# Performance work log

Measured on AMD Instinct MI355X. Metric: run time of the kernel, lower is better.

The kernel has to match this reference:

```python
import jax, jax.numpy as jnp
import numpy as np

N = 40000
E = 200000
D = 32
NUM_BANDS = 3
ORDER = 4
EPS = 1e-8
LN_EPS = 1e-5


def setup_inputs() -> dict:
    key = jax.random.key(0)
    ks = jax.random.split(key, 20)
    h = jax.random.normal(ks[0], (N, D), dtype=jnp.float32)
    Q = jax.random.normal(ks[1], (E, D, D), dtype=jnp.float32) / jnp.sqrt(jnp.float32(D))
    edge_index = jax.random.randint(ks[2], (2, E), 0, N, dtype=jnp.int32)
    coeffs = jnp.ones((NUM_BANDS, ORDER + 1), dtype=jnp.float32) / (ORDER + 1)
    s = 1.0 / np.sqrt(D)
    proj_W = jax.random.uniform(ks[3], (NUM_BANDS, D, D), minval=-s, maxval=s, dtype=jnp.float32)
    proj_b = jax.random.uniform(ks[4], (NUM_BANDS, D), minval=-s, maxval=s, dtype=jnp.float32)
    proj_g = jnp.ones((NUM_BANDS, D), dtype=jnp.float32)
    proj_beta = jnp.zeros((NUM_BANDS, D), dtype=jnp.float32)
    s3 = 1.0 / np.sqrt(NUM_BANDS * D)
    fus_W1 = jax.random.uniform(ks[5], (NUM_BANDS * D, D), minval=-s3, maxval=s3, dtype=jnp.float32)
    fus_b1 = jax.random.uniform(ks[6], (D,), minval=-s3, maxval=s3, dtype=jnp.float32)
    fus_g = jnp.ones((D,), dtype=jnp.float32)
    fus_beta = jnp.zeros((D,), dtype=jnp.float32)
    fus_W2 = jax.random.uniform(ks[7], (D, D), minval=-s, maxval=s, dtype=jnp.float32)
    fus_b2 = jax.random.uniform(ks[8], (D,), minval=-s, maxval=s, dtype=jnp.float32)
    return {"h": h, "Q": Q, "edge_index": edge_index, "coeffs": coeffs,
            "proj_W": proj_W, "proj_b": proj_b, "proj_g": proj_g, "proj_beta": proj_beta,
            "fus_W1": fus_W1, "fus_b1": fus_b1, "fus_g": fus_g, "fus_beta": fus_beta,
            "fus_W2": fus_W2, "fus_b2": fus_b2}


def _layer_norm(x, g, b):
    mu = x.mean(-1, keepdims=True)
    var = x.var(-1, keepdims=True)  # biased, as torch LayerNorm
    return (x - mu) / jnp.sqrt(var + LN_EPS) * g + b


def reference(h, Q, edge_index, coeffs, proj_W, proj_b, proj_g, proj_beta,
              fus_W1, fus_b1, fus_g, fus_beta, fus_W2, fus_b2):
    row, col = edge_index[0], edge_index[1]
    n = h.shape[0]
    ones_e = jnp.ones(row.shape[0], dtype=h.dtype)
    deg = (jax.ops.segment_sum(ones_e, row, num_segments=n)
           + jax.ops.segment_sum(ones_e, col, num_segments=n))  # [N]

    def matvec(x):
        # gather -> per-edge DxD bmm -> scatter_add; diag via degree
        Qh = jnp.einsum('eij,ej->ei', Q, x[col])          # [E, D]
        off = jax.ops.segment_sum(Qh, row, num_segments=n)  # [N, D]
        return deg[:, None] * x - off

    # power iteration for lambda_max (5 iters, fixed key for determinism)
    v = jax.random.normal(jax.random.key(42), h.shape, dtype=h.dtype)
    v = v / jnp.linalg.norm(v)
    lam = jnp.array(1.0, dtype=h.dtype)
    for _ in range(5):
        Lv = matvec(v)
        lam = (v * Lv).sum() / ((v * v).sum() + EPS)
        v = Lv / (jnp.linalg.norm(Lv) + EPS)
    lam = jnp.maximum(lam, 1.0)

    def L_tilde(x):
        return 2.0 / (lam + EPS) * matvec(x) - x

    bands = []
    for b_idx in range(NUM_BANDS):
        w = jax.nn.softmax(coeffs[b_idx])
        T_prev = h
        T_curr = L_tilde(h)
        res = w[0] * T_prev + w[1] * T_curr
        for k in range(2, ORDER + 1):
            T_next = 2.0 * L_tilde(T_curr) - T_prev
            res = res + w[k] * T_next
            T_prev, T_curr = T_curr, T_next
        p = jax.nn.silu(_layer_norm(res @ proj_W[b_idx] + proj_b[b_idx],
                                    proj_g[b_idx], proj_beta[b_idx]))
        bands.append(p)

    cat = jnp.concatenate(bands, axis=-1)  # [N, 3D]
    fused = jax.nn.silu(_layer_norm(cat @ fus_W1 + fus_b1, fus_g, fus_beta)) @ fus_W2 + fus_b2
    return h + fused
```

## Files before the change

### kernel.cpp

```cpp
#include <hip/hip_runtime.h>
#include <hip/hip_fp16.h>
#include <math.h>

#define NN 40000
#define EE 200000
#define DD 32
#define ND (NN * DD)
#define LNEPS 1e-5f

typedef float    fv4 __attribute__((ext_vector_type(4)));
typedef unsigned uv4 __attribute__((ext_vector_type(4)));

#define SLOT_S1    0
#define SLOT_S2    32
#define SLOT_ALPHA 48

__device__ __forceinline__ void threefry2x32(unsigned k0, unsigned k1,
                                             unsigned x0, unsigned x1,
                                             unsigned& o0, unsigned& o1) {
  const unsigned k2 = k0 ^ k1 ^ 0x1BD11BDAu;
  unsigned v0 = x0 + k0, v1 = x1 + k1;
#define TF_ROUND(r) { v0 += v1; v1 = (v1 << (r)) | (v1 >> (32 - (r))); v1 ^= v0; }
  TF_ROUND(13) TF_ROUND(15) TF_ROUND(26) TF_ROUND(6)
  v0 += k1; v1 += k2 + 1u;
  TF_ROUND(17) TF_ROUND(29) TF_ROUND(16) TF_ROUND(24)
  v0 += k2; v1 += k0 + 2u;
  TF_ROUND(13) TF_ROUND(15) TF_ROUND(26) TF_ROUND(6)
  v0 += k0; v1 += k1 + 3u;
  TF_ROUND(17) TF_ROUND(29) TF_ROUND(16) TF_ROUND(24)
  v0 += k1; v1 += k2 + 4u;
  TF_ROUND(13) TF_ROUND(15) TF_ROUND(26) TF_ROUND(6)
  v0 += k2; v1 += k0 + 5u;
#undef TF_ROUND
  o0 = v0; o1 = v1;
}

__device__ __forceinline__ float wave64_sum(float x) {
  for (int o = 32; o > 0; o >>= 1) x += __shfl_xor(x, o, 64);
  return x;
}
__device__ __forceinline__ float g32_sum(float x) {
  for (int o = 16; o > 0; o >>= 1) x += __shfl_xor(x, o, 32);
  return x;
}

__global__ void k_deg(const int* __restrict__ ei, float* __restrict__ deg,
                      int* __restrict__ hist) {
  int e = blockIdx.x * 256 + threadIdx.x;
  if (e < EE) {
    int r = ei[e];
    atomicAdd(deg + r, 1.0f);
    atomicAdd(deg + ei[EE + e], 1.0f);
    atomicAdd(hist + r, 1);
  }
}

__global__ __launch_bounds__(1024) void k_scan(const int* __restrict__ hist,
                                               int* __restrict__ row_start,
                                               int* __restrict__ cursor) {
  __shared__ int part[1024];
  const int t = threadIdx.x;
  const int base = t * 40;
  int s = 0;
  for (int i = base; i < base + 40 && i < NN; ++i) s += hist[i];
  part[t] = s;
  __syncthreads();
  for (int off = 1; off < 1024; off <<= 1) {
    int v = (t >= off) ? part[t - off] : 0;
    __syncthreads();
    part[t] += v;
    __syncthreads();
  }
  int ex = (t == 0) ? 0 : part[t - 1];
  for (int i = base; i < base + 40 && i < NN; ++i) {
    row_start[i] = ex;
    cursor[i] = ex;
    ex += hist[i];
  }
  if (t == 0) row_start[NN] = EE;
}

__global__ void k_genv(float* __restrict__ v) {
  int i = blockIdx.x * 256 + threadIdx.x;
  unsigned o0, o1;
  threefry2x32(0u, 42u, 0u, (unsigned)i, o0, o1);
  unsigned bits = o1;
  float f = __uint_as_float((bits >> 9) | 0x3f800000u) - 1.0f;
  const float lo = -0.99999994f;
  float u = fmaxf(lo, f * 2.0f + lo);
  v[i] = 1.41421354f * erfinvf(u);
}

__device__ __forceinline__ int clamp8(float q) {
  int v = (int)rintf(q);
  return v < -127 ? -127 : (v > 127 ? 127 : v);
}
__device__ __forceinline__ unsigned pack4v(fv4 q, float inv) {
  int q0 = clamp8(q.x * inv), q1 = clamp8(q.y * inv),
      q2 = clamp8(q.z * inv), q3 = clamp8(q.w * inv);
  return (q0 & 255) | ((q1 & 255) << 8) | ((q2 & 255) << 16) | ((q3 & 255) << 24);
}
__device__ __forceinline__ void dp4(unsigned u, fv4 xv, float& acc) {
  acc = fmaf((float)(signed char)(u),        xv.x, acc);
  acc = fmaf((float)(signed char)(u >> 8),   xv.y, acc);
  acc = fmaf((float)(signed char)(u >> 16),  xv.z, acc);
  acc = fmaf((float)(signed char)(u >> 24),  xv.w, acc);
}

__global__ __launch_bounds__(256) void k_cvt(const float* __restrict__ Q,
                                             const int* __restrict__ ei,
                                             int* __restrict__ cursor,
                                             char* __restrict__ Qi8,
                                             __half* __restrict__ Qs,
                                             int* __restrict__ cols) {
  const int slot = threadIdx.x >> 5;
  const int lane = threadIdx.x & 31;
  const int e = blockIdx.x * 8 + slot;
  const int row = ei[e];
  const int col = ei[EE + e];
  int pos = 0;
  if (lane == 0) pos = atomicAdd(cursor + row, 1);
  pos = __shfl(pos, 0, 32);
  const fv4* __restrict__ q4 =
      (const fv4*)(Q + (size_t)e * (DD * DD) + (size_t)lane * DD);
  fv4 qf[8];
#pragma unroll
  for (int k = 0; k < 8; ++k) qf[k] = __builtin_nontemporal_load(q4 + k);
  float m = 0.0f;
#pragma unroll
  for (int k = 0; k < 8; ++k) {
    m = fmaxf(m, fmaxf(fmaxf(fabsf(qf[k].x), fabsf(qf[k].y)),
                       fmaxf(fabsf(qf[k].z), fabsf(qf[k].w))));
  }
  __half sh = __float2half(m * (1.0f / 127.0f));
  float s = __half2float(sh);
  float inv = (s > 0.0f) ? 1.0f / s : 0.0f;
  uv4 pa, pb;
  pa.x = pack4v(qf[0], inv); pa.y = pack4v(qf[1], inv);
  pa.z = pack4v(qf[2], inv); pa.w = pack4v(qf[3], inv);
  pb.x = pack4v(qf[4], inv); pb.y = pack4v(qf[5], inv);
  pb.z = pack4v(qf[6], inv); pb.w = pack4v(qf[7], inv);
  uv4* __restrict__ qs = (uv4*)(Qi8 + (size_t)pos * (DD * DD) + (size_t)lane * DD);
  qs[0] = pa;
  qs[1] = pb;
  Qs[pos * DD + lane] = sh;
  if (lane == 0) cols[pos] = col;
}

#define CHUNK 16

__global__ __launch_bounds__(256) void k_gather(const float* __restrict__ x,
                                                const float* __restrict__ xprev,
                                                const char* __restrict__ Qi8,
                                                const __half* __restrict__ Qs,
                                                const int* __restrict__ cols,
                                                const int* __restrict__ row_start,
                                                const float* __restrict__ deg,
                                                const float* __restrict__ scal,
                                                float* __restrict__ out, int mode) {
  __shared__ float lds[4][CHUNK][DD];
  const int wid  = threadIdx.x >> 6;
  const int lane = threadIdx.x & 63;
  const int half = lane >> 5;
  const int d    = lane & 31;
  const int r = blockIdx.x * 4 + wid;
  const int beg = row_start[r];
  const int end = row_start[r + 1];
  const int degree = end - beg;

  float acc = 0.0f;
  for (int chunk = 0; chunk < degree; chunk += CHUNK) {
    const int nchunk = min(CHUNK, degree - chunk);
    int myc = (lane < nchunk) ? cols[beg + chunk + lane] : 0;
    {
      const int el = lane >> 2;
      const int pt = lane & 3;
      if (el < nchunk) {
        const int c = __shfl(myc, el, 64);
        const fv4* __restrict__ xs = (const fv4*)(x + (size_t)c * DD);
        fv4 a = xs[pt * 2];
        fv4 b = xs[pt * 2 + 1];
        fv4* __restrict__ dst = (fv4*)&lds[wid][el][pt * 8];
        dst[0] = a;
        dst[1] = b;
      }
    }
    uv4 qa = {0, 0, 0, 0}, qb = {0, 0, 0, 0};
    float sc = 0.0f;
    {
      const int p = half;
      if (p < nchunk) {
        const size_t pos = (size_t)(beg + chunk + p);
        const uv4* __restrict__ q8 = (const uv4*)(Qi8 + pos * (DD * DD) + (size_t)d * DD);
        qa = q8[0];
        qb = q8[1];
        sc = __half2float(Qs[pos * DD + d]);
      }
    }
    for (int p0 = 0; p0 < nchunk; p0 += 2) {
      const int pn = p0 + 2 + half;
      uv4 na = {0, 0, 0, 0}, nb = {0, 0, 0, 0};
      float ns = 0.0f;
      if (pn < nchunk) {
        const size_t pos = (size_t)(beg + chunk + pn);
        const uv4* __restrict__ q8 = (const uv4*)(Qi8 + pos * (DD * DD) + (size_t)d * DD);
        na = q8[0];
        nb = q8[1];
        ns = __half2float(Qs[pos * DD + d]);
      }
      const int p = p0 + half;
      if (p < nchunk) {
        const fv4* __restrict__ xl = (const fv4*)&lds[wid][p][0];
        fv4 xr[8];
#pragma unroll
        for (int k = 0; k < 8; ++k) xr[k] = xl[k];
        float dot = 0.0f;
        dp4(qa.x, xr[0], dot); dp4(qa.y, xr[1], dot);
        dp4(qa.z, xr[2], dot); dp4(qa.w, xr[3], dot);
        dp4(qb.x, xr[4], dot); dp4(qb.y, xr[5], dot);
        dp4(qb.z, xr[6], dot); dp4(qb.w, xr[7], dot);
        acc = fmaf(sc, dot, acc);
      }
      qa = na; qb = nb; sc = ns;
    }
  }
  acc += __shfl_xor(acc, 32, 64);

  if (half == 0) {
    const size_t idx = (size_t)r * DD + d;
    const float xi = x[idx];
    const float dv = deg[r];
    float o;
    if (mode == 0)      o = dv * xi - acc;
    else if (mode == 1) o = scal[SLOT_ALPHA] * (dv * xi - acc) - xi;
    else                o = 2.0f * scal[SLOT_ALPHA] * (dv * xi - acc)
                            - 2.0f * xi - xprev[idx];
    out[idx] = o;
  }
}

__global__ void k_pre(const float* __restrict__ x, const float* __restrict__ xprev,
                      const float* __restrict__ deg, const float* __restrict__ scal,
                      float* __restrict__ out, int mode) {
  int i = blockIdx.x * 256 + threadIdx.x;
  float d = deg[i >> 5];
  float xi = x[i];
  if (mode == 0)       out[i] = d * xi;
  else if (mode == 1)  out[i] = scal[SLOT_ALPHA] * d * xi - xi;
  else                 out[i] = 2.0f * scal[SLOT_ALPHA] * d * xi - 2.0f * xi - xprev[i];
}

__global__ __launch_bounds__(256) void k_matvec(const float* __restrict__ x,
                                                const float* __restrict__ Q,
                                                const int* __restrict__ ei,
                                                float* __restrict__ out,
                                                const float* __restrict__ scal,
                                                int use_alpha, float smul) {
  const int slot = threadIdx.x >> 5;
  const int lane = threadIdx.x & 31;
  const int e = blockIdx.x * 8 + slot;
  const float factor = use_alpha ? scal[SLOT_ALPHA] * smul : smul;
  const int row = ei[e];
  const int col = ei[EE + e];
  const fv4* __restrict__ x4 = (const fv4*)(x + (size_t)col * DD);
  fv4 xr[8];
#pragma unroll
  for (int k = 0; k < 8; ++k) xr[k] = x4[k];
  const fv4* __restrict__ q4 =
      (const fv4*)(Q + (size_t)e * (DD * DD) + (size_t)lane * DD);
  float acc = 0.0f;
#pragma unroll
  for (int k = 0; k < 8; ++k) {
    fv4 q = q4[k];
    acc = fmaf(q.x, xr[k].x, acc);
    acc = fmaf(q.y, xr[k].y, acc);
    acc = fmaf(q.z, xr[k].z, acc);
    acc = fmaf(q.w, xr[k].w, acc);
  }
  atomicAdd(out + (size_t)row * DD + lane, -factor * acc);
}

#define DOT_BLOCKS 640
__global__ void k_dots(const float* __restrict__ u4, const float* __restrict__ u5,
                       float* __restrict__ scal) {
  float s1 = 0.0f, s2 = 0.0f;
  for (int i = blockIdx.x * 256 + threadIdx.x; i < ND; i += DOT_BLOCKS * 256) {
    float a = u4[i], b = u5[i];
    s1 = fmaf(a, b, s1);
    s2 = fmaf(a, a, s2);
  }
  s1 = wave64_sum(s1);
  s2 = wave64_sum(s2);
  __shared__ float ls1[4], ls2[4];
  int w = threadIdx.x >> 6;
  if ((threadIdx.x & 63) == 0) { ls1[w] = s1; ls2[w] = s2; }
  __syncthreads();
  if (threadIdx.x == 0) {
    atomicAdd(scal + SLOT_S1, ls1[0] + ls1[1] + ls1[2] + ls1[3]);
    atomicAdd(scal + SLOT_S2, ls2[0] + ls2[1] + ls2[2] + ls2[3]);
  }
}

__global__ void k_alpha(float* __restrict__ scal) {
  float lam = scal[SLOT_S1] / scal[SLOT_S2] / (1.0f + 1e-8f);
  lam = fmaxf(lam, 1.0f);
  scal[SLOT_ALPHA] = 2.0f / (lam + 1e-8f);
}

__global__ __launch_bounds__(256) void k_fuse(
    const float* __restrict__ h,
    const float* __restrict__ T1, const float* __restrict__ T2,
    const float* __restrict__ T3, const float* __restrict__ T4,
    const float* __restrict__ coeffs,
    const float* __restrict__ projW, const float* __restrict__ projb,
    const float* __restrict__ projg, const float* __restrict__ projbeta,
    const float* __restrict__ fusW1, const float* __restrict__ fusb1,
    const float* __restrict__ fusg, const float* __restrict__ fusbeta,
    const float* __restrict__ fusW2, const float* __restrict__ fusb2,
    float* __restrict__ out) {
  __shared__ float s_res[8][3][DD];
  __shared__ float s_p[8][3 * DD];
  __shared__ float s_s[8][DD];
  const int slot = threadIdx.x >> 5;
  const int lane = threadIdx.x & 31;
  const int n = blockIdx.x * 8 + slot;

  float w[3][5];
#pragma unroll
  for (int b = 0; b < 3; ++b) {
    float m = -1e30f;
#pragma unroll
    for (int k = 0; k < 5; ++k) m = fmaxf(m, coeffs[b * 5 + k]);
    float s = 0.0f;
#pragma unroll
    for (int k = 0; k < 5; ++k) { w[b][k] = expf(coeffs[b * 5 + k] - m); s += w[b][k]; }
#pragma unroll
    for (int k = 0; k < 5; ++k) w[b][k] /= s;
  }

  const int idx = n * DD + lane;
  float hd = h[idx], t1 = T1[idx], t2 = T2[idx], t3 = T3[idx], t4 = T4[idx];
#pragma unroll
  for (int b = 0; b < 3; ++b)
    s_res[slot][b][lane] =
        w[b][0] * hd + w[b][1] * t1 + w[b][2] * t2 + w[b][3] * t3 + w[b][4] * t4;
  __syncthreads();

#pragma unroll
  for (int b = 0; b < 3; ++b) {
    float y = projb[b * DD + lane];
#pragma unroll
    for (int j = 0; j < DD; ++j)
      y = fmaf(s_res[slot][b][j], projW[(b * DD + j) * DD + lane], y);
    float mu = g32_sum(y) * (1.0f / DD);
    float d = y - mu;
    float var = g32_sum(d * d) * (1.0f / DD);
    float z = d * rsqrtf(var + LNEPS) * projg[b * DD + lane] + projbeta[b * DD + lane];
    float pb = z / (1.0f + expf(-z));
    s_p[slot][b * DD + lane] = pb;
  }
  __syncthreads();

  float y = fusb1[lane];
#pragma unroll
  for (int j = 0; j < 3 * DD; ++j)
    y = fmaf(s_p[slot][j], fusW1[j * DD + lane], y);
  float mu = g32_sum(y) * (1.0f / DD);
  float d = y - mu;
  float var = g32_sum(d * d) * (1.0f / DD);
  float z = d * rsqrtf(var + LNEPS) * fusg[lane] + fusbeta[lane];
  float sv = z / (1.0f + expf(-z));
  s_s[slot][lane] = sv;
  __syncthreads();

  float o = fusb2[lane];
#pragma unroll
  for (int j = 0; j < DD; ++j)
    o = fmaf(s_s[slot][j], fusW2[j * DD + lane], o);
  out[idx] = hd + o;
}

extern "C" void kernel_launch(void* const* d_in, const int* in_sizes, int n_in,
                              void* d_out, int out_size, void* d_ws, size_t ws_size,
                              hipStream_t stream) {
  (void)in_sizes; (void)n_in; (void)out_size;
  const float* h        = (const float*)d_in[0];
  const float* Q        = (const float*)d_in[1];
  const int*   ei       = (const int*)d_in[2];
  const float* coeffs   = (const float*)d_in[3];
  const float* projW    = (const float*)d_in[4];
  const float* projb    = (const float*)d_in[5];
  const float* projg    = (const float*)d_in[6];
  const float* projbeta = (const float*)d_in[7];
  const float* fusW1    = (const float*)d_in[8];
  const float* fusb1    = (const float*)d_in[9];
  const float* fusg     = (const float*)d_in[10];
  const float* fusbeta  = (const float*)d_in[11];
  const float* fusW2    = (const float*)d_in[12];
  const float* fusb2    = (const float*)d_in[13];
  float* out = (float*)d_out;

  const size_t qi_bytes  = (size_t)EE * DD * DD;
  const size_t qs_bytes  = (size_t)EE * DD * sizeof(__half);
  const size_t col_bytes = (size_t)EE * sizeof(int);
  const size_t idx_bytes = (size_t)(3 * NN + 2) * sizeof(int);
  const size_t f32_elems = 6u * (size_t)ND + NN + 64;
  const size_t need = qi_bytes + qs_bytes + col_bytes + idx_bytes +
                      f32_elems * sizeof(float) + 256;
  const bool fast = ws_size >= need;

  char*   Qi8 = (char*)d_ws;
  __half* Qs  = (__half*)((char*)d_ws + qi_bytes);
  int*  cols      = (int*)((char*)d_ws + qi_bytes + qs_bytes);
  int*  row_start = cols + EE;
  int*  cursor    = row_start + NN + 1;
  float* base = fast
      ? (float*)((char*)d_ws + ((qi_bytes + qs_bytes + col_bytes + idx_bytes + 255) & ~(size_t)255))
      : (float*)d_ws;
  float* uA   = base;
  float* uB   = uA + ND;
  float* T1   = uB + ND;
  float* T2   = T1 + ND;
  float* T3   = T2 + ND;
  float* T4   = T3 + ND;
  float* deg  = T4 + ND;
  float* scal = deg + NN;
  int*   hist = (int*)(scal + 64);

  (void)hipMemsetAsync(deg, 0, (2 * NN + 64) * sizeof(float), stream);

  k_deg<<<(EE + 255) / 256, 256, 0, stream>>>(ei, deg, hist);
  k_genv<<<ND / 256, 256, 0, stream>>>(uA);

  if (fast) {
    k_scan<<<1, 1024, 0, stream>>>(hist, row_start, cursor);
    k_cvt<<<EE / 8, 256, 0, stream>>>(Q, ei, cursor, Qi8, Qs, cols);

    float* cur = uA;
    float* nxt = uB;
    for (int it = 0; it < 5; ++it) {
      k_gather<<<NN / 4, 256, 0, stream>>>(cur, nullptr, Qi8, Qs, cols,
                                           row_start, deg, scal, nxt, 0);
      float* t = cur; cur = nxt; nxt = t;
    }
    k_dots<<<DOT_BLOCKS, 256, 0, stream>>>(nxt, cur, scal);
    k_alpha<<<1, 1, 0, stream>>>(scal);

    const float* xin[4]   = {h, T1, T2, T3};
    const float* prevs[4] = {nullptr, h, T1, T2};
    float* touts[4]       = {T1, T2, T3, T4};
    for (int k = 0; k < 4; ++k) {
      k_gather<<<NN / 4, 256, 0, stream>>>(xin[k], prevs[k], Qi8, Qs, cols,
                                           row_start, deg, scal, touts[k],
                                           k == 0 ? 1 : 2);
    }
  } else {
    float* cur = uA;
    float* nxt = uB;
    for (int it = 0; it < 5; ++it) {
      k_pre<<<ND / 256, 256, 0, stream>>>(cur, nullptr, deg, scal, nxt, 0);
      k_matvec<<<EE / 8, 256, 0, stream>>>(cur, Q, ei, nxt, scal, 0, 1.0f);
      float* t = cur; cur = nxt; nxt = t;
    }
    k_dots<<<DOT_BLOCKS, 256, 0, stream>>>(nxt, cur, scal);
    k_alpha<<<1, 1, 0, stream>>>(scal);
    const float* xin[4]   = {h, T1, T2, T3};
    const float* prevs[4] = {nullptr, h, T1, T2};
    float* touts[4]       = {T1, T2, T3, T4};
    for (int k = 0; k < 4; ++k) {
      k_pre<<<ND / 256, 256, 0, stream>>>(xin[k], prevs[k], deg, scal, touts[k],
                                          k == 0 ? 1 : 2);
      k_matvec<<<EE / 8, 256, 0, stream>>>(xin[k], Q, ei, touts[k], scal, 1,
                                           k == 0 ? 1.0f : 2.0f);
    }
  }

  k_fuse<<<NN / 8, 256, 0, stream>>>(h, T1, T2, T3, T4, coeffs,
                                     projW, projb, projg, projbeta,
                                     fusW1, fusb1, fusg, fusbeta,
                                     fusW2, fusb2, out);
}
```

Before: 950.9 us.

## Fuse power iteration and Chebyshev sweeps into persistent kernels with grid barriers

Replaces eleven separate gather launches plus the dot and alpha kernels with two persistent kernels of 1024 blocks. Each kernel loops over rows in a grid-stride pattern and separates dependent sweeps with a hierarchical atomic grid barrier. The dot-product reduction and lambda computation are folded into the power kernel. This removes launch overhead and tail idle time between passes, but requires all 1024 blocks to be co-resident, adds spin-wait barrier cost, and the barrier gives up after a fixed spin count instead of failing.

```diff
diff --git a/kernel.cpp b/kernel.cpp
--- a/kernel.cpp
+++ b/kernel.cpp
@@ -7,13 +7,13 @@
 #define DD 32
 #define ND (NN * DD)
 #define LNEPS 1e-5f
+#define GRID 1024
 
 typedef float    fv4 __attribute__((ext_vector_type(4)));
 typedef unsigned uv4 __attribute__((ext_vector_type(4)));
 
-#define SLOT_S1    0
-#define SLOT_S2    32
 #define SLOT_ALPHA 48
+#define SCAL_FLOATS (64 + 2048 + 64)
 
 __device__ __forceinline__ void threefry2x32(unsigned k0, unsigned k1,
                                              unsigned x0, unsigned x1,
@@ -44,6 +44,41 @@
   return x;
 }
 
+__device__ __forceinline__ void gbar(int* bar) {
+  __syncthreads();
+  if (threadIdx.x == 0) {
+    __threadfence();
+    int* gen = bar + 33 * 32;
+    int g = __hip_atomic_load(gen, __ATOMIC_RELAXED, __HIP_MEMORY_SCOPE_AGENT);
+    const int leaf = blockIdx.x & 31;
+    int c = __hip_atomic_fetch_add(bar + leaf * 32, 1, __ATOMIC_ACQ_REL,
+                                   __HIP_MEMORY_SCOPE_AGENT);
+    bool done = false;
+    if (c == (GRID / 32) - 1) {
+      __hip_atomic_store(bar + leaf * 32, 0, __ATOMIC_RELAXED,
+                         __HIP_MEMORY_SCOPE_AGENT);
+      int rc = __hip_atomic_fetch_add(bar + 32 * 32, 1, __ATOMIC_ACQ_REL,
+                                      __HIP_MEMORY_SCOPE_AGENT);
+      if (rc == 31) {
+        __hip_atomic_store(bar + 32 * 32, 0, __ATOMIC_RELAXED,
+                           __HIP_MEMORY_SCOPE_AGENT);
+        __hip_atomic_store(gen, g + 1, __ATOMIC_RELEASE,
+                           __HIP_MEMORY_SCOPE_AGENT);
+        done = true;
+      }
+    }
+    if (!done) {
+      long long spins = 0;
+      while (__hip_atomic_load(gen, __ATOMIC_ACQUIRE,
+                               __HIP_MEMORY_SCOPE_AGENT) == g) {
+        __builtin_amdgcn_s_sleep(2);
+        if (++spins > 200000000LL) break;
+      }
+    }
+  }
+  __syncthreads();
+}
+
 __global__ void k_deg(const int* __restrict__ ei, float* __restrict__ deg,
                       int* __restrict__ hist) {
   int e = blockIdx.x * 256 + threadIdx.x;
@@ -149,93 +184,175 @@
 
 #define CHUNK 16
 
-__global__ __launch_bounds__(256) void k_gather(const float* __restrict__ x,
-                                                const float* __restrict__ xprev,
-                                                const char* __restrict__ Qi8,
-                                                const __half* __restrict__ Qs,
-                                                const int* __restrict__ cols,
-                                                const int* __restrict__ row_start,
-                                                const float* __restrict__ deg,
-                                                const float* __restrict__ scal,
-                                                float* __restrict__ out, int mode) {
-  __shared__ float lds[4][CHUNK][DD];
-  const int wid  = threadIdx.x >> 6;
+__device__ __forceinline__ void sweep_rows(const float* __restrict__ x,
+                                           const float* __restrict__ xprev,
+                                           const char* __restrict__ Qi8,
+                                           const __half* __restrict__ Qs,
+                                           const int* __restrict__ cols,
+                                           const int* __restrict__ row_start,
+                                           const float* __restrict__ deg,
+                                           float alpha,
+                                           float* __restrict__ out, int mode,
+                                           float (*ldsw)[DD]) {
   const int lane = threadIdx.x & 63;
   const int half = lane >> 5;
   const int d    = lane & 31;
-  const int r = blockIdx.x * 4 + wid;
-  const int beg = row_start[r];
-  const int end = row_start[r + 1];
-  const int degree = end - beg;
-
-  float acc = 0.0f;
-  for (int chunk = 0; chunk < degree; chunk += CHUNK) {
-    const int nchunk = min(CHUNK, degree - chunk);
-    int myc = (lane < nchunk) ? cols[beg + chunk + lane] : 0;
-    {
-      const int el = lane >> 2;
-      const int pt = lane & 3;
-      if (el < nchunk) {
-        const int c = __shfl(myc, el, 64);
-        const fv4* __restrict__ xs = (const fv4*)(x + (size_t)c * DD);
-        fv4 a = xs[pt * 2];
-        fv4 b = xs[pt * 2 + 1];
-        fv4* __restrict__ dst = (fv4*)&lds[wid][el][pt * 8];
-        dst[0] = a;
-        dst[1] = b;
+  const int wid  = threadIdx.x >> 6;
+  for (int r = blockIdx.x * 4 + wid; r < NN; r += GRID * 4) {
+    const int beg = row_start[r];
+    const int end = row_start[r + 1];
+    const int degree = end - beg;
+    float acc = 0.0f;
+    for (int chunk = 0; chunk < degree; chunk += CHUNK) {
+      const int nchunk = min(CHUNK, degree - chunk);
+      int myc = (lane < nchunk) ? cols[beg + chunk + lane] : 0;
+      {
+        const int el = lane >> 2;
+        const int pt = lane & 3;
+        if (el < nchunk) {
+          const int c = __shfl(myc, el, 64);
+          const fv4* __restrict__ xs = (const fv4*)(x + (size_t)c * DD);
+          fv4 a = xs[pt * 2];
+          fv4 b = xs[pt * 2 + 1];
+          fv4* __restrict__ dst = (fv4*)&ldsw[el][pt * 8];
+          dst[0] = a;
+          dst[1] = b;
+        }
       }
-    }
-    uv4 qa = {0, 0, 0, 0}, qb = {0, 0, 0, 0};
-    float sc = 0.0f;
-    {
-      const int p = half;
-      if (p < nchunk) {
-        const size_t pos = (size_t)(beg + chunk + p);
-        const uv4* __restrict__ q8 = (const uv4*)(Qi8 + pos * (DD * DD) + (size_t)d * DD);
-        qa = q8[0];
-        qb = q8[1];
-        sc = __half2float(Qs[pos * DD + d]);
+      uv4 qa = {0, 0, 0, 0}, qb = {0, 0, 0, 0};
+      float sc = 0.0f;
+      {
+        const int p = half;
+        if (p < nchunk) {
+          const size_t pos = (size_t)(beg + chunk + p);
+          const uv4* __restrict__ q8 =
+              (const uv4*)(Qi8 + pos * (DD * DD) + (size_t)d * DD);
+          qa = q8[0];
+          qb = q8[1];
+          sc = __half2float(Qs[pos * DD + d]);
+        }
       }
-    }
-    for (int p0 = 0; p0 < nchunk; p0 += 2) {
-      const int pn = p0 + 2 + half;
-      uv4 na = {0, 0, 0, 0}, nb = {0, 0, 0, 0};
-      float ns = 0.0f;
-      if (pn < nchunk) {
-        const size_t pos = (size_t)(beg + chunk + pn);
-        const uv4* __restrict__ q8 = (const uv4*)(Qi8 + pos * (DD * DD) + (size_t)d * DD);
-        na = q8[0];
-        nb = q8[1];
-        ns = __half2float(Qs[pos * DD + d]);
+      for (int p0 = 0; p0 < nchunk; p0 += 2) {
+        const int pn = p0 + 2 + half;
+        uv4 na = {0, 0, 0, 0}, nb = {0, 0, 0, 0};
+        float ns = 0.0f;
+        if (pn < nchunk) {
+          const size_t pos = (size_t)(beg + chunk + pn);
+          const uv4* __restrict__ q8 =
+              (const uv4*)(Qi8 + pos * (DD * DD) + (size_t)d * DD);
+          na = q8[0];
+          nb = q8[1];
+          ns = __half2float(Qs[pos * DD + d]);
+        }
+        const int p = p0 + half;
+        if (p < nchunk) {
+          const fv4* __restrict__ xl = (const fv4*)&ldsw[p][0];
+          fv4 xr[8];
+#pragma unroll
+          for (int k = 0; k < 8; ++k) xr[k] = xl[k];
+          float dot = 0.0f;
+          dp4(qa.x, xr[0], dot); dp4(qa.y, xr[1], dot);
+          dp4(qa.z, xr[2], dot); dp4(qa.w, xr[3], dot);
+          dp4(qb.x, xr[4], dot); dp4(qb.y, xr[5], dot);
+          dp4(qb.z, xr[6], dot); dp4(qb.w, xr[7], dot);
+          acc = fmaf(sc, dot, acc);
+        }
+        qa = na; qb = nb; sc = ns;
       }
-      const int p = p0 + half;
-      if (p < nchunk) {
-        const fv4* __restrict__ xl = (const fv4*)&lds[wid][p][0];
-        fv4 xr[8];
-#pragma unroll
-        for (int k = 0; k < 8; ++k) xr[k] = xl[k];
-        float dot = 0.0f;
-        dp4(qa.x, xr[0], dot); dp4(qa.y, xr[1], dot);
-        dp4(qa.z, xr[2], dot); dp4(qa.w, xr[3], dot);
-        dp4(qb.x, xr[4], dot); dp4(qb.y, xr[5], dot);
-        dp4(qb.z, xr[6], dot); dp4(qb.w, xr[7], dot);
-        acc = fmaf(sc, dot, acc);
-      }
-      qa = na; qb = nb; sc = ns;
-    }
-  }
-  acc += __shfl_xor(acc, 32, 64);
-
-  if (half == 0) {
-    const size_t idx = (size_t)r * DD + d;
-    const float xi = x[idx];
-    const float dv = deg[r];
-    float o;
-    if (mode == 0)      o = dv * xi - acc;
-    else if (mode == 1) o = scal[SLOT_ALPHA] * (dv * xi - acc) - xi;
-    else                o = 2.0f * scal[SLOT_ALPHA] * (dv * xi - acc)
-                            - 2.0f * xi - xprev[idx];
-    out[idx] = o;
+    }
+    acc += __shfl_xor(acc, 32, 64);
+    if (half == 0) {
+      const size_t idx = (size_t)r * DD + d;
+      const float xi = x[idx];
+      const float dv = deg[r];
+      float o;
+      if (mode == 0)      o = dv * xi - acc;
+      else if (mode == 1) o = alpha * (dv * xi - acc) - xi;
+      else                o = 2.0f * alpha * (dv * xi - acc) - 2.0f * xi - xprev[idx];
+      out[idx] = o;
+    }
+  }
+}
+
+__global__ __launch_bounds__(256, 4) void k_power(const char* __restrict__ Qi8,
+                                                  const __half* __restrict__ Qs,
+                                                  const int* __restrict__ cols,
+                                                  const int* __restrict__ row_start,
+                                                  const float* __restrict__ deg,
+                                                  float* __restrict__ uA,
+                                                  float* __restrict__ uB,
+                                                  float* __restrict__ scal,
+                                                  int* __restrict__ bar) {
+  __shared__ float lds[4][CHUNK][DD];
+  float (*ldsw)[DD] = lds[threadIdx.x >> 6];
+
+  const float* src[5] = {uA, uB, uA, uB, uA};
+  float*       dst[5] = {uB, uA, uB, uA, uB};
+#pragma unroll
+  for (int s = 0; s < 5; ++s) {
+    sweep_rows(src[s], uA, Qi8, Qs, cols, row_start, deg, 0.0f, dst[s], 0, ldsw);
+    gbar(bar);
+  }
+  float s1 = 0.0f, s2 = 0.0f;
+  for (int i = blockIdx.x * 256 + threadIdx.x; i < ND; i += GRID * 256) {
+    float a = uA[i], b = uB[i];
+    s1 = fmaf(a, b, s1);
+    s2 = fmaf(a, a, s2);
+  }
+  s1 = wave64_sum(s1);
+  s2 = wave64_sum(s2);
+  __shared__ float ls1[4], ls2[4];
+  int w = threadIdx.x >> 6;
+  if ((threadIdx.x & 63) == 0) { ls1[w] = s1; ls2[w] = s2; }
+  __syncthreads();
+  if (threadIdx.x == 0) {
+    const int leaf = blockIdx.x & 31;
+    float b1 = ls1[0] + ls1[1] + ls1[2] + ls1[3];
+    float b2 = ls2[0] + ls2[1] + ls2[2] + ls2[3];
+    __hip_atomic_fetch_add(scal + 64 + leaf * 32, b1, __ATOMIC_RELAXED,
+                           __HIP_MEMORY_SCOPE_AGENT);
+    __hip_atomic_fetch_add(scal + 64 + 1024 + leaf * 32, b2, __ATOMIC_RELAXED,
+                           __HIP_MEMORY_SCOPE_AGENT);
+  }
+  gbar(bar);
+  if (blockIdx.x == 0 && threadIdx.x == 0) {
+    float S1 = 0.0f, S2 = 0.0f;
+    for (int l = 0; l < 32; ++l) {
+      S1 += __hip_atomic_load(scal + 64 + l * 32, __ATOMIC_ACQUIRE,
+                              __HIP_MEMORY_SCOPE_AGENT);
+      S2 += __hip_atomic_load(scal + 64 + 1024 + l * 32, __ATOMIC_ACQUIRE,
+                              __HIP_MEMORY_SCOPE_AGENT);
+    }
+    float lam = S1 / S2 / (1.0f + 1e-8f);
+    lam = fmaxf(lam, 1.0f);
+    scal[SLOT_ALPHA] = 2.0f / (lam + 1e-8f);
+  }
+}
+
+__global__ __launch_bounds__(256, 4) void k_cheb4(const float* __restrict__ h,
+                                                  const char* __restrict__ Qi8,
+                                                  const __half* __restrict__ Qs,
+                                                  const int* __restrict__ cols,
+                                                  const int* __restrict__ row_start,
+                                                  const float* __restrict__ deg,
+                                                  const float* __restrict__ scal,
+                                                  float* __restrict__ T1,
+                                                  float* __restrict__ T2,
+                                                  float* __restrict__ T3,
+                                                  float* __restrict__ T4,
+                                                  int* __restrict__ bar) {
+  __shared__ float lds[4][CHUNK][DD];
+  float (*ldsw)[DD] = lds[threadIdx.x >> 6];
+  const float alpha = scal[SLOT_ALPHA];
+
+  const float* xin[4] = {h, T1, T2, T3};
+  const float* prv[4] = {h, h, T1, T2};
+  float*      outs[4] = {T1, T2, T3, T4};
+#pragma unroll
+  for (int k = 0; k < 4; ++k) {
+    sweep_rows(xin[k], prv[k], Qi8, Qs, cols, row_start, deg, alpha, outs[k],
+               k == 0 ? 1 : 2, ldsw);
+    if (k < 3) gbar(bar);
   }
 }
 
@@ -296,13 +413,13 @@
   if ((threadIdx.x & 63) == 0) { ls1[w] = s1; ls2[w] = s2; }
   __syncthreads();
   if (threadIdx.x == 0) {
-    atomicAdd(scal + SLOT_S1, ls1[0] + ls1[1] + ls1[2] + ls1[3]);
-    atomicAdd(scal + SLOT_S2, ls2[0] + ls2[1] + ls2[2] + ls2[3]);
+    atomicAdd(scal + 64, ls1[0] + ls1[1] + ls1[2] + ls1[3]);
+    atomicAdd(scal + 64 + 1024, ls2[0] + ls2[1] + ls2[2] + ls2[3]);
   }
 }
 
 __global__ void k_alpha(float* __restrict__ scal) {
-  float lam = scal[SLOT_S1] / scal[SLOT_S2] / (1.0f + 1e-8f);
+  float lam = scal[64] / scal[64 + 1024] / (1.0f + 1e-8f);
   lam = fmaxf(lam, 1.0f);
   scal[SLOT_ALPHA] = 2.0f / (lam + 1e-8f);
 }
@@ -404,9 +521,10 @@
   const size_t qs_bytes  = (size_t)EE * DD * sizeof(__half);
   const size_t col_bytes = (size_t)EE * sizeof(int);
   const size_t idx_bytes = (size_t)(3 * NN + 2) * sizeof(int);
-  const size_t f32_elems = 6u * (size_t)ND + NN + 64;
-  const size_t need = qi_bytes + qs_bytes + col_bytes + idx_bytes +
-                      f32_elems * sizeof(float) + 256;
+  const size_t BAR_INTS  = 34 * 32 + 64;
+  const size_t f32_elems = 6u * (size_t)ND + NN + SCAL_FLOATS;
+  const size_t meta = qi_bytes + qs_bytes + col_bytes + idx_bytes;
+  const size_t need = meta + (f32_elems + NN + BAR_INTS) * sizeof(float) + 512;
   const bool fast = ws_size >= need;
 
   char*   Qi8 = (char*)d_ws;
@@ -415,7 +533,7 @@
   int*  row_start = cols + EE;
   int*  cursor    = row_start + NN + 1;
   float* base = fast
-      ? (float*)((char*)d_ws + ((qi_bytes + qs_bytes + col_bytes + idx_bytes + 255) & ~(size_t)255))
+      ? (float*)((char*)d_ws + ((meta + 255) & ~(size_t)255))
       : (float*)d_ws;
   float* uA   = base;
   float* uB   = uA + ND;
@@ -425,9 +543,12 @@
   float* T4   = T3 + ND;
   float* deg  = T4 + ND;
   float* scal = deg + NN;
-  int*   hist = (int*)(scal + 64);
-
-  (void)hipMemsetAsync(deg, 0, (2 * NN + 64) * sizeof(float), stream);
+  int*   hist = (int*)(scal + SCAL_FLOATS);
+  int*   bar  = hist + NN;
+
+  (void)hipMemsetAsync(deg, 0,
+                       (2 * (size_t)NN + SCAL_FLOATS + BAR_INTS) * sizeof(float),
+                       stream);
 
   k_deg<<<(EE + 255) / 256, 256, 0, stream>>>(ei, deg, hist);
   k_genv<<<ND / 256, 256, 0, stream>>>(uA);
@@ -435,25 +556,10 @@
   if (fast) {
     k_scan<<<1, 1024, 0, stream>>>(hist, row_start, cursor);
     k_cvt<<<EE / 8, 256, 0, stream>>>(Q, ei, cursor, Qi8, Qs, cols);
-
-    float* cur = uA;
-    float* nxt = uB;
-    for (int it = 0; it < 5; ++it) {
-      k_gather<<<NN / 4, 256, 0, stream>>>(cur, nullptr, Qi8, Qs, cols,
-                                           row_start, deg, scal, nxt, 0);
-      float* t = cur; cur = nxt; nxt = t;
-    }
-    k_dots<<<DOT_BLOCKS, 256, 0, stream>>>(nxt, cur, scal);
-    k_alpha<<<1, 1, 0, stream>>>(scal);
-
-    const float* xin[4]   = {h, T1, T2, T3};
-    const float* prevs[4] = {nullptr, h, T1, T2};
-    float* touts[4]       = {T1, T2, T3, T4};
-    for (int k = 0; k < 4; ++k) {
-      k_gather<<<NN / 4, 256, 0, stream>>>(xin[k], prevs[k], Qi8, Qs, cols,
-                                           row_start, deg, scal, touts[k],
-                                           k == 0 ? 1 : 2);
-    }
+    k_power<<<GRID, 256, 0, stream>>>(Qi8, Qs, cols, row_start, deg, uA, uB,
+                                      scal, bar);
+    k_cheb4<<<GRID, 256, 0, stream>>>(h, Qi8, Qs, cols, row_start, deg, scal,
+                                      T1, T2, T3, T4, bar);
   } else {
     float* cur = uA;
     float* nxt = uB;
```

Result: slower. 2.288 ms (+140.6%).

## Fuse first power-iteration matvec into Q quantization pass and deepen Q prefetch

Applied to the files above, without the earlier changes.

The first power-iteration matvec is computed inside the Q conversion kernel using the fp32 Q already loaded, scattering results with atomics into a buffer pre-initialized by k_pre. This removes one gather pass over the quantized Q. The gather kernel now prefetches Q two edges ahead and hoists per-row loads before the loop. The cost is extra x gathers and atomics in the conversion kernel, plus higher register pressure in the gather.

```diff
diff --git a/kernel.cpp b/kernel.cpp
--- a/kernel.cpp
+++ b/kernel.cpp
@@ -107,12 +107,14 @@
   acc = fmaf((float)(signed char)(u >> 24),  xv.w, acc);
 }
 
-__global__ __launch_bounds__(256) void k_cvt(const float* __restrict__ Q,
-                                             const int* __restrict__ ei,
-                                             int* __restrict__ cursor,
-                                             char* __restrict__ Qi8,
-                                             __half* __restrict__ Qs,
-                                             int* __restrict__ cols) {
+__global__ __launch_bounds__(256) void k_cvt_mv(const float* __restrict__ x,
+                                                const float* __restrict__ Q,
+                                                const int* __restrict__ ei,
+                                                int* __restrict__ cursor,
+                                                char* __restrict__ Qi8,
+                                                __half* __restrict__ Qs,
+                                                int* __restrict__ cols,
+                                                float* __restrict__ out) {
   const int slot = threadIdx.x >> 5;
   const int lane = threadIdx.x & 31;
   const int e = blockIdx.x * 8 + slot;
@@ -121,11 +123,23 @@
   int pos = 0;
   if (lane == 0) pos = atomicAdd(cursor + row, 1);
   pos = __shfl(pos, 0, 32);
+  const fv4* __restrict__ x4 = (const fv4*)(x + (size_t)col * DD);
+  fv4 xr[8];
+#pragma unroll
+  for (int k = 0; k < 8; ++k) xr[k] = x4[k];
   const fv4* __restrict__ q4 =
       (const fv4*)(Q + (size_t)e * (DD * DD) + (size_t)lane * DD);
   fv4 qf[8];
 #pragma unroll
   for (int k = 0; k < 8; ++k) qf[k] = __builtin_nontemporal_load(q4 + k);
+  float acc = 0.0f;
+#pragma unroll
+  for (int k = 0; k < 8; ++k) {
+    acc = fmaf(qf[k].x, xr[k].x, acc);
+    acc = fmaf(qf[k].y, xr[k].y, acc);
+    acc = fmaf(qf[k].z, xr[k].z, acc);
+    acc = fmaf(qf[k].w, xr[k].w, acc);
+  }
   float m = 0.0f;
 #pragma unroll
   for (int k = 0; k < 8; ++k) {
@@ -145,6 +159,7 @@
   qs[1] = pb;
   Qs[pos * DD + lane] = sh;
   if (lane == 0) cols[pos] = col;
+  atomicAdd(out + (size_t)row * DD + lane, -acc);
 }
 
 #define CHUNK 16
@@ -168,6 +183,11 @@
   const int end = row_start[r + 1];
   const int degree = end - beg;
 
+  const size_t idx = (size_t)r * DD + d;
+  const float xi = x[idx];
+  const float dv = deg[r];
+  const float xp = (mode == 2) ? xprev[idx] : 0.0f;
+
   float acc = 0.0f;
   for (int chunk = 0; chunk < degree; chunk += CHUNK) {
     const int nchunk = min(CHUNK, degree - chunk);
@@ -185,29 +205,22 @@
         dst[1] = b;
       }
     }
-    uv4 qa = {0, 0, 0, 0}, qb = {0, 0, 0, 0};
-    float sc = 0.0f;
-    {
-      const int p = half;
-      if (p < nchunk) {
-        const size_t pos = (size_t)(beg + chunk + p);
-        const uv4* __restrict__ q8 = (const uv4*)(Qi8 + pos * (DD * DD) + (size_t)d * DD);
-        qa = q8[0];
-        qb = q8[1];
-        sc = __half2float(Qs[pos * DD + d]);
-      }
-    }
+    uv4 a0 = {0,0,0,0}, b0 = {0,0,0,0}, a1 = {0,0,0,0}, b1 = {0,0,0,0};
+    float s0 = 0.0f, s1 = 0.0f;
+#define LOADQ(PP, A, B, S)                                                    \
+    if ((PP) < nchunk) {                                                      \
+      const size_t pos = (size_t)(beg + chunk + (PP));                        \
+      const uv4* __restrict__ q8 =                                            \
+          (const uv4*)(Qi8 + pos * (DD * DD) + (size_t)d * DD);               \
+      A = q8[0]; B = q8[1];                                                   \
+      S = __half2float(Qs[pos * DD + d]);                                     \
+    }
+    LOADQ(half, a0, b0, s0)
+    LOADQ(2 + half, a1, b1, s1)
     for (int p0 = 0; p0 < nchunk; p0 += 2) {
-      const int pn = p0 + 2 + half;
-      uv4 na = {0, 0, 0, 0}, nb = {0, 0, 0, 0};
-      float ns = 0.0f;
-      if (pn < nchunk) {
-        const size_t pos = (size_t)(beg + chunk + pn);
-        const uv4* __restrict__ q8 = (const uv4*)(Qi8 + pos * (DD * DD) + (size_t)d * DD);
-        na = q8[0];
-        nb = q8[1];
-        ns = __half2float(Qs[pos * DD + d]);
-      }
+      uv4 a2 = {0,0,0,0}, b2 = {0,0,0,0};
+      float s2 = 0.0f;
+      LOADQ(p0 + 4 + half, a2, b2, s2)
       const int p = p0 + half;
       if (p < nchunk) {
         const fv4* __restrict__ xl = (const fv4*)&lds[wid][p][0];
@@ -215,26 +228,25 @@
 #pragma unroll
         for (int k = 0; k < 8; ++k) xr[k] = xl[k];
         float dot = 0.0f;
-        dp4(qa.x, xr[0], dot); dp4(qa.y, xr[1], dot);
-        dp4(qa.z, xr[2], dot); dp4(qa.w, xr[3], dot);
-        dp4(qb.x, xr[4], dot); dp4(qb.y, xr[5], dot);
-        dp4(qb.z, xr[6], dot); dp4(qb.w, xr[7], dot);
-        acc = fmaf(sc, dot, acc);
+        dp4(a0.x, xr[0], dot); dp4(a0.y, xr[1], dot);
+        dp4(a0.z, xr[2], dot); dp4(a0.w, xr[3], dot);
+        dp4(b0.x, xr[4], dot); dp4(b0.y, xr[5], dot);
+        dp4(b0.z, xr[6], dot); dp4(b0.w, xr[7], dot);
+        acc = fmaf(s0, dot, acc);
       }
-      qa = na; qb = nb; sc = ns;
-    }
+      a0 = a1; b0 = b1; s0 = s1;
+      a1 = a2; b1 = b2; s1 = s2;
+    }
+#undef LOADQ
   }
   acc += __shfl_xor(acc, 32, 64);
 
   if (half == 0) {
-    const size_t idx = (size_t)r * DD + d;
-    const float xi = x[idx];
-    const float dv = deg[r];
     float o;
     if (mode == 0)      o = dv * xi - acc;
     else if (mode == 1) o = scal[SLOT_ALPHA] * (dv * xi - acc) - xi;
     else                o = 2.0f * scal[SLOT_ALPHA] * (dv * xi - acc)
-                            - 2.0f * xi - xprev[idx];
+                            - 2.0f * xi - xp;
     out[idx] = o;
   }
 }
@@ -404,9 +416,9 @@
   const size_t qs_bytes  = (size_t)EE * DD * sizeof(__half);
   const size_t col_bytes = (size_t)EE * sizeof(int);
   const size_t idx_bytes = (size_t)(3 * NN + 2) * sizeof(int);
-  const size_t f32_elems = 6u * (size_t)ND + NN + 64;
-  const size_t need = qi_bytes + qs_bytes + col_bytes + idx_bytes +
-                      f32_elems * sizeof(float) + 256;
+  const size_t f32_elems = 6u * (size_t)ND + 2u * NN + 64;
+  const size_t meta = qi_bytes + qs_bytes + col_bytes + idx_bytes;
+  const size_t need = meta + f32_elems * sizeof(float) + 512;
   const bool fast = ws_size >= need;
 
   char*   Qi8 = (char*)d_ws;
@@ -415,7 +427,7 @@
   int*  row_start = cols + EE;
   int*  cursor    = row_start + NN + 1;
   float* base = fast
-      ? (float*)((char*)d_ws + ((qi_bytes + qs_bytes + col_bytes + idx_bytes + 255) & ~(size_t)255))
+      ? (float*)((char*)d_ws + ((meta + 255) & ~(size_t)255))
       : (float*)d_ws;
   float* uA   = base;
   float* uB   = uA + ND;
@@ -427,27 +439,29 @@
   float* scal = deg + NN;
   int*   hist = (int*)(scal + 64);
 
-  (void)hipMemsetAsync(deg, 0, (2 * NN + 64) * sizeof(float), stream);
+  (void)hipMemsetAsync(deg, 0, (2 * (size_t)NN + 64) * sizeof(float), stream);
 
   k_deg<<<(EE + 255) / 256, 256, 0, stream>>>(ei, deg, hist);
   k_genv<<<ND / 256, 256, 0, stream>>>(uA);
 
   if (fast) {
     k_scan<<<1, 1024, 0, stream>>>(hist, row_start, cursor);
-    k_cvt<<<EE / 8, 256, 0, stream>>>(Q, ei, cursor, Qi8, Qs, cols);
-
-    float* cur = uA;
-    float* nxt = uB;
-    for (int it = 0; it < 5; ++it) {
-      k_gather<<<NN / 4, 256, 0, stream>>>(cur, nullptr, Qi8, Qs, cols,
-                                           row_start, deg, scal, nxt, 0);
-      float* t = cur; cur = nxt; nxt = t;
-    }
-    k_dots<<<DOT_BLOCKS, 256, 0, stream>>>(nxt, cur, scal);
+    k_pre<<<ND / 256, 256, 0, stream>>>(uA, nullptr, deg, scal, uB, 0);
+    k_cvt_mv<<<EE / 8, 256, 0, stream>>>(uA, Q, ei, cursor, Qi8, Qs, cols, uB);
+
+    k_gather<<<NN / 4, 256, 0, stream>>>(uB, nullptr, Qi8, Qs, cols,
+                                         row_start, deg, scal, uA, 0);
+    k_gather<<<NN / 4, 256, 0, stream>>>(uA, nullptr, Qi8, Qs, cols,
+                                         row_start, deg, scal, uB, 0);
+    k_gather<<<NN / 4, 256, 0, stream>>>(uB, nullptr, Qi8, Qs, cols,
+                                         row_start, deg, scal, uA, 0);
+    k_gather<<<NN / 4, 256, 0, stream>>>(uA, nullptr, Qi8, Qs, cols,
+                                         row_start, deg, scal, uB, 0);
+    k_dots<<<DOT_BLOCKS, 256, 0, stream>>>(uA, uB, scal);
     k_alpha<<<1, 1, 0, stream>>>(scal);
 
     const float* xin[4]   = {h, T1, T2, T3};
-    const float* prevs[4] = {nullptr, h, T1, T2};
+    const float* prevs[4] = {h, h, T1, T2};
     float* touts[4]       = {T1, T2, T3, T4};
     for (int k = 0; k < 4; ++k) {
       k_gather<<<NN / 4, 256, 0, stream>>>(xin[k], prevs[k], Qi8, Qs, cols,
```

Measured after the change: 944.2 us. Within noise of the previous version (-0.7%).
